# Kernel optimization log

Measured on AMD Instinct MI355X. Metric: run time of the kernel, lower is better.

The kernel has to match this reference:

```python
import jax, jax.numpy as jnp
import numpy as np

E, T, D, H = 4, 4096, 2048, 8192

def setup_inputs() -> dict:
    key = jax.random.key(0)
    k1, k2, k3 = jax.random.split(key, 3)
    x = jax.random.normal(k1, (E, T, D), dtype=jnp.float32)
    fc1_w = jax.random.normal(k2, (E, D, H), dtype=jnp.float32) * 0.001
    fc2_w = jax.random.normal(k3, (E, H, D), dtype=jnp.float32) * 0.001
    fc1_b = jnp.zeros((E, 1, H), dtype=jnp.float32)
    fc2_b = jnp.zeros((E, 1, D), dtype=jnp.float32)
    return {"x": x, "fc1_w": fc1_w, "fc1_b": fc1_b, "fc2_w": fc2_w, "fc2_b": fc2_b}

def reference(x, fc1_w, fc1_b, fc2_w, fc2_b):
    # batched expert FFN: y = relu(x @ W1 + b1) @ W2 + b2, per expert e
    y = jnp.einsum('etd,edh->eth', x, fc1_w) + fc1_b
    y = jax.nn.relu(y)
    y = jnp.einsum('eth,ehd->etd', y, fc2_w) + fc2_b
    return y
```

## Files before the change

### kernel.cpp

```cpp
#include <hip/hip_runtime.h>
#include <hip/hip_bf16.h>
#include <stdint.h>

#define E_ 4
#define T_ 4096
#define D_ 2048
#define H_ 8192

typedef __attribute__((ext_vector_type(8))) short bf16x8;
typedef __attribute__((ext_vector_type(4))) float f32x4;

__device__ __forceinline__ unsigned short f2bf(float f) {
    unsigned int u = __float_as_uint(f);
    u = u + 0x7fffu + ((u >> 16) & 1u);
    return (unsigned short)(u >> 16);
}

__device__ __forceinline__ void async16(const unsigned short* g, unsigned short* l) {
    auto gp = (const __attribute__((address_space(1))) unsigned int*)g;
    auto lp = (__attribute__((address_space(3))) unsigned int*)l;
    __builtin_amdgcn_global_load_lds(gp, lp, 16 , 0 , 0 );
}

__device__ __forceinline__ f32x4 mfma16(bf16x8 a, bf16x8 b, f32x4 c) {
    return __builtin_amdgcn_mfma_f32_16x16x32_bf16(a, b, c, 0, 0, 0);
}

__global__ void cvt_x_kernel(const float4* __restrict__ in, uint2* __restrict__ out, long n4) {
    long i = (long)blockIdx.x * blockDim.x + threadIdx.x;
    long stride = (long)gridDim.x * blockDim.x;
    for (; i < n4; i += stride) {
        float4 v = in[i];
        uint2 o;
        o.x = (unsigned)f2bf(v.x) | ((unsigned)f2bf(v.y) << 16);
        o.y = (unsigned)f2bf(v.z) | ((unsigned)f2bf(v.w) << 16);
        out[i] = o;
    }
}

__global__ void transpose_cvt_kernel(const float* __restrict__ W, unsigned short* __restrict__ Wt,
                                     int R, int C) {
    __shared__ float tile[64][65];
    const float* Wp = W + (size_t)blockIdx.z * R * C;
    unsigned short* Wtp = Wt + (size_t)blockIdx.z * R * C;
    const int c0 = blockIdx.x * 64, r0 = blockIdx.y * 64;
    const int tc = threadIdx.x & 63;
    const int tr = threadIdx.x >> 6;
#pragma unroll
    for (int i = 0; i < 16; ++i) {
        int r = tr * 16 + i;
        tile[r][tc] = Wp[(size_t)(r0 + r) * C + c0 + tc];
    }
    __syncthreads();
#pragma unroll
    for (int i = 0; i < 16; ++i) {
        int r = tr * 16 + i;
        Wtp[(size_t)(c0 + r) * R + r0 + tc] = f2bf(tile[tc][r]);
    }
}

template <int K, int OUT_MODE>
__global__ __launch_bounds__(512, 2) void gemm256_kernel(
    const unsigned short* __restrict__ A,
    const unsigned short* __restrict__ Bt,
    const float* __restrict__ bias,
    void* __restrict__ Cout,
    int M, int N)
{
    constexpr int BK = 64;
    constexpr int NT = K / BK;
    __shared__ __align__(16) unsigned short L[2][2][2][128][64];

    const int nx = gridDim.x, ny = gridDim.y;
    const int nwg = nx * ny * gridDim.z;
    const int w = (blockIdx.z * ny + blockIdx.y) * nx + blockIdx.x;
    const int cpx = nwg >> 3;
    const int lid = (w & 7) * cpx + (w >> 3);
    const int e  = lid / (nx * ny);
    const int r2 = lid % (nx * ny);
    const int by = r2 / nx, bx = r2 % nx;

    const unsigned short* Ae = A + (size_t)e * M * K;
    const unsigned short* Be = Bt + (size_t)e * N * K;
    const int bm0 = by * 256;
    const int bn0 = bx * 256;

    const int tid = threadIdx.x;
    const int lane = tid & 63;
    const int wid = tid >> 6;
    const int wr = wid >> 2;
    const int wc = wid & 3;

    const int srow = wid * 16 + (lane >> 3);
    const int skel = 8 * ((lane & 7) ^ (lane >> 3));

    const int fr = lane & 15;
    const int kq = lane >> 4;
    const int ksw = (lane & 7) << 3;
    const int bh = wc >> 1;
    const int brb = (wc & 1) * 64;

    f32x4 acc[8][4] = {};

    auto stageA = [&](int t, int h) {
        const int k0 = t * BK;
        const int s = t & 1;
#pragma unroll
        for (int i = 0; i < 2; ++i) {
            async16(Ae + (size_t)(bm0 + h * 128 + srow + i * 8) * K + k0 + skel,
                    &L[s][0][h][wid * 16 + i * 8][0]);
        }
    };
    auto stageB = [&](int t, int h) {
        const int k0 = t * BK;
        const int s = t & 1;
#pragma unroll
        for (int i = 0; i < 2; ++i) {
            async16(Be + (size_t)(bn0 + h * 128 + srow + i * 8) * K + k0 + skel,
                    &L[s][1][h][wid * 16 + i * 8][0]);
        }
    };

    stageB(0, 0); stageB(0, 1); stageA(0, 0); stageA(0, 1);
    stageB(1, 0); stageB(1, 1); stageA(1, 0); stageA(1, 1);

    bf16x8 a[4][2], b[4][2];

    for (int t = 0; t < NT; ++t) {
        const int s = t & 1;

        if (t == NT - 1) {
            asm volatile("s_waitcnt vmcnt(0)" ::: "memory");
        } else {
            asm volatile("s_waitcnt vmcnt(8)" ::: "memory");
        }
        __builtin_amdgcn_s_barrier();

#pragma unroll
        for (int n = 0; n < 2; ++n)
#pragma unroll
            for (int kk = 0; kk < 2; ++kk)
                b[n][kk] = *(const bf16x8*)&L[s][1][bh][brb + n * 16 + fr][(kk * 32 + kq * 8) ^ ksw];
#pragma unroll
        for (int m = 0; m < 4; ++m)
#pragma unroll
            for (int kk = 0; kk < 2; ++kk)
                a[m][kk] = *(const bf16x8*)&L[s][0][wr][m * 16 + fr][(kk * 32 + kq * 8) ^ ksw];
#pragma unroll
        for (int n = 2; n < 4; ++n)
#pragma unroll
            for (int kk = 0; kk < 2; ++kk)
                b[n][kk] = *(const bf16x8*)&L[s][1][bh][brb + n * 16 + fr][(kk * 32 + kq * 8) ^ ksw];

        __builtin_amdgcn_s_setprio(1);
#pragma unroll
        for (int m = 0; m < 4; ++m)
#pragma unroll
            for (int n = 0; n < 4; ++n)
#pragma unroll
                for (int kk = 0; kk < 2; ++kk)
                    acc[m][n] = mfma16(a[m][kk], b[n][kk], acc[m][n]);
        __builtin_amdgcn_s_setprio(0);

#pragma unroll
        for (int m = 0; m < 4; ++m)
#pragma unroll
            for (int kk = 0; kk < 2; ++kk)
                a[m][kk] = *(const bf16x8*)&L[s][0][wr][(m + 4) * 16 + fr][(kk * 32 + kq * 8) ^ ksw];

        asm volatile("s_waitcnt lgkmcnt(0)" ::: "memory");
        __builtin_amdgcn_s_barrier();

        if (t + 2 < NT) {
            stageB(t + 2, 0); stageB(t + 2, 1);
            stageA(t + 2, 0); stageA(t + 2, 1);
        }
        __builtin_amdgcn_sched_barrier(0);

        __builtin_amdgcn_s_setprio(1);
#pragma unroll
        for (int m = 0; m < 4; ++m)
#pragma unroll
            for (int n = 0; n < 4; ++n)
#pragma unroll
                for (int kk = 0; kk < 2; ++kk)
                    acc[m + 4][n] = mfma16(a[m][kk], b[n][kk], acc[m + 4][n]);
        __builtin_amdgcn_s_setprio(0);
    }

    const int rowq = (lane >> 4) * 4;
    const float* bp = bias + (size_t)e * N;

    if (OUT_MODE == 0) {
        unsigned short* Y = (unsigned short*)Cout + (size_t)e * M * N;
#pragma unroll
        for (int n = 0; n < 4; ++n) {
            const int cg = bn0 + wc * 64 + n * 16 + fr;
            const float bb = bp[cg];
#pragma unroll
            for (int m = 0; m < 8; ++m) {
                const int rg0 = bm0 + wr * 128 + m * 16 + rowq;
#pragma unroll
                for (int j = 0; j < 4; ++j) {
                    float v = acc[m][n][j] + bb;
                    v = fmaxf(v, 0.0f);
                    Y[(size_t)(rg0 + j) * N + cg] = f2bf(v);
                }
            }
        }
    } else {
        float* O = (float*)Cout + (size_t)e * M * N;
#pragma unroll
        for (int n = 0; n < 4; ++n) {
            const int cg = bn0 + wc * 64 + n * 16 + fr;
            const float bb = bp[cg];
#pragma unroll
            for (int m = 0; m < 8; ++m) {
                const int rg0 = bm0 + wr * 128 + m * 16 + rowq;
#pragma unroll
                for (int j = 0; j < 4; ++j) {
                    O[(size_t)(rg0 + j) * N + cg] = acc[m][n][j] + bb;
                }
            }
        }
    }
}

extern "C" void kernel_launch(void* const* d_in, const int* in_sizes, int n_in,
                              void* d_out, int out_size, void* d_ws, size_t ws_size,
                              hipStream_t stream) {
    const float* x     = (const float*)d_in[0];
    const float* fc1_w = (const float*)d_in[1];
    const float* fc1_b = (const float*)d_in[2];
    const float* fc2_w = (const float*)d_in[3];
    const float* fc2_b = (const float*)d_in[4];
    float* out = (float*)d_out;

    const size_t n_x  = (size_t)E_ * T_ * D_;
    const size_t n_w1 = (size_t)E_ * D_ * H_;
    const size_t n_w2 = (size_t)E_ * H_ * D_;
    const size_t n_y1 = (size_t)E_ * T_ * H_;

    const size_t need = (n_x + n_w1 + n_w2 + n_y1) * sizeof(unsigned short);
    if (ws_size < need) return;

    unsigned short* xb  = (unsigned short*)d_ws;
    unsigned short* w1t = xb + n_x;
    unsigned short* w2t = w1t + n_w1;
    unsigned short* y1  = w2t + n_w2;

    cvt_x_kernel<<<2048, 256, 0, stream>>>((const float4*)x, (uint2*)xb, (long)(n_x / 4));
    {
        dim3 g(H_ / 64, D_ / 64, E_);
        transpose_cvt_kernel<<<g, 256, 0, stream>>>(fc1_w, w1t, D_, H_);
    }
    {
        dim3 g(D_ / 64, H_ / 64, E_);
        transpose_cvt_kernel<<<g, 256, 0, stream>>>(fc2_w, w2t, H_, D_);
    }
    {
        dim3 g(H_ / 256, T_ / 256, E_);
        gemm256_kernel<D_, 0><<<g, 512, 0, stream>>>(xb, w1t, fc1_b, (void*)y1, T_, H_);
    }
    {
        dim3 g(D_ / 256, T_ / 256, E_);
        gemm256_kernel<H_, 1><<<g, 512, 0, stream>>>(y1, w2t, fc2_b, (void*)out, T_, D_);
    }
}
```

Baseline: 1.210 ms.

## Stage GEMM epilogue through LDS for coalesced stores and remap tile order

The epilogue now writes accumulators to shared memory in 32-row slices and reads them back so each lane stores 4 contiguous output elements, replacing scattered 2- or 4-byte column stores with vectorized row-contiguous writes. The workgroup-to-tile mapping also changes: each XCD gets a contiguous band of row tiles, walked in column groups of 16, to improve L2 reuse of A/B panels. A sched_barrier is added before the mid-loop barrier. The staged epilogue adds eight block-wide syncs and extra LDS traffic per tile.

```diff
diff --git a/kernel.cpp b/kernel.cpp
--- a/kernel.cpp
+++ b/kernel.cpp
@@ -9,6 +9,7 @@
 
 typedef __attribute__((ext_vector_type(8))) short bf16x8;
 typedef __attribute__((ext_vector_type(4))) float f32x4;
+typedef __attribute__((ext_vector_type(4))) unsigned short u16x4;
 
 __device__ __forceinline__ unsigned short f2bf(float f) {
     unsigned int u = __float_as_uint(f);
@@ -75,10 +76,18 @@
     const int nwg = nx * ny * gridDim.z;
     const int w = (blockIdx.z * ny + blockIdx.y) * nx + blockIdx.x;
     const int cpx = nwg >> 3;
-    const int lid = (w & 7) * cpx + (w >> 3);
-    const int e  = lid / (nx * ny);
-    const int r2 = lid % (nx * ny);
-    const int by = r2 / nx, bx = r2 % nx;
+    const int xcd = w & 7;
+    const int c = w >> 3;
+    const int CR = cpx / nx;
+    const int GX = (nx % 16 == 0) ? 16 : nx;
+    const int g = c / (GX * CR);
+    const int r1 = c - g * (GX * CR);
+    const int byl = r1 / GX;
+    const int bxi = r1 - byl * GX;
+    const int fy = xcd * CR + byl;
+    const int bx = g * GX + bxi;
+    const int e = fy / ny;
+    const int by = fy - e * ny;
 
     const unsigned short* Ae = A + (size_t)e * M * K;
     const unsigned short* Be = Bt + (size_t)e * N * K;
@@ -169,6 +178,7 @@
                 a[m][kk] = *(const bf16x8*)&L[s][0][wr][(m + 4) * 16 + fr][(kk * 32 + kq * 8) ^ ksw];
 
         asm volatile("s_waitcnt lgkmcnt(0)" ::: "memory");
+        __builtin_amdgcn_sched_barrier(0);
         __builtin_amdgcn_s_barrier();
 
         if (t + 2 < NT) {
@@ -188,39 +198,48 @@
         __builtin_amdgcn_s_setprio(0);
     }
 
+    constexpr int ST = 260;
+    float* S = (float*)&L[0][0][0][0][0];
     const int rowq = (lane >> 4) * 4;
     const float* bp = bias + (size_t)e * N;
-
-    if (OUT_MODE == 0) {
-        unsigned short* Y = (unsigned short*)Cout + (size_t)e * M * N;
-#pragma unroll
-        for (int n = 0; n < 4; ++n) {
-            const int cg = bn0 + wc * 64 + n * 16 + fr;
-            const float bb = bp[cg];
-#pragma unroll
-            for (int m = 0; m < 8; ++m) {
-                const int rg0 = bm0 + wr * 128 + m * 16 + rowq;
-#pragma unroll
-                for (int j = 0; j < 4; ++j) {
-                    float v = acc[m][n][j] + bb;
-                    v = fmaxf(v, 0.0f);
-                    Y[(size_t)(rg0 + j) * N + cg] = f2bf(v);
+    const float4 bb4 = *(const float4*)(bp + bn0 + lane * 4);
+
+    unsigned short* Y = (unsigned short*)Cout + (size_t)e * M * N;
+    float* O = (float*)Cout + (size_t)e * M * N;
+
+#pragma unroll
+    for (int s = 0; s < 8; ++s) {
+        __syncthreads();
+        if (wr == (s >> 2)) {
+            const int sl = s & 3;
+#pragma unroll
+            for (int mm = 0; mm < 2; ++mm) {
+#pragma unroll
+                for (int n = 0; n < 4; ++n) {
+#pragma unroll
+                    for (int j = 0; j < 4; ++j) {
+                        S[(mm * 16 + rowq + j) * ST + wc * 64 + n * 16 + fr] =
+                            acc[2 * sl + mm][n][j];
+                    }
                 }
             }
         }
-    } else {
-        float* O = (float*)Cout + (size_t)e * M * N;
-#pragma unroll
-        for (int n = 0; n < 4; ++n) {
-            const int cg = bn0 + wc * 64 + n * 16 + fr;
-            const float bb = bp[cg];
-#pragma unroll
-            for (int m = 0; m < 8; ++m) {
-                const int rg0 = bm0 + wr * 128 + m * 16 + rowq;
-#pragma unroll
-                for (int j = 0; j < 4; ++j) {
-                    O[(size_t)(rg0 + j) * N + cg] = acc[m][n][j] + bb;
-                }
+        __syncthreads();
+#pragma unroll
+        for (int rr = 0; rr < 4; ++rr) {
+            const int rl = wid * 4 + rr;
+            const int rg = bm0 + s * 32 + rl;
+            f32x4 v = *(const f32x4*)&S[rl * ST + lane * 4];
+            v[0] += bb4.x; v[1] += bb4.y; v[2] += bb4.z; v[3] += bb4.w;
+            if (OUT_MODE == 0) {
+                u16x4 o;
+                o[0] = f2bf(fmaxf(v[0], 0.0f));
+                o[1] = f2bf(fmaxf(v[1], 0.0f));
+                o[2] = f2bf(fmaxf(v[2], 0.0f));
+                o[3] = f2bf(fmaxf(v[3], 0.0f));
+                *(u16x4*)(Y + (size_t)rg * N + bn0 + lane * 4) = o;
+            } else {
+                *(f32x4*)(O + (size_t)rg * N + bn0 + lane * 4) = v;
             }
         }
     }
```

Measured after the change: 1.160 ms. 4.1% less time.
